# Kernel optimization log

Hardware: AMD Instinct MI355X
Metric: run time of the kernel (lower is better)

## Reference

```python
import jax, jax.numpy as jnp
import numpy as np

B, S, H = 2, 2048, 2048
NH, G = 16, 4
HD = H // NH  # 128


def setup_inputs() -> dict:
    key = jax.random.key(0)
    ks = jax.random.split(key, 9)
    sc = 0.02
    x = jax.random.normal(ks[0], (B, S, H), dtype=jnp.float32)
    # causal mask: 1.0 where j > i (masked), added as mask * -1e9 (matches torch code)
    causal_mask = jnp.triu(jnp.ones((S, S), dtype=jnp.float32), k=1)[None, None]
    Wq = jax.random.normal(ks[1], (H, H), dtype=jnp.float32) * sc
    bq = jnp.zeros((H,), dtype=jnp.float32)
    Wk = jax.random.normal(ks[2], (H, G * HD), dtype=jnp.float32) * sc
    bk = jnp.zeros((G * HD,), dtype=jnp.float32)
    Wv = jax.random.normal(ks[3], (H, G * HD), dtype=jnp.float32) * sc
    bv = jnp.zeros((G * HD,), dtype=jnp.float32)
    Wo = jax.random.normal(ks[4], (H, H), dtype=jnp.float32) * sc
    bo = jnp.zeros((H,), dtype=jnp.float32)
    return {"hidden_state": x, "causal_mask": causal_mask,
            "Wq": Wq, "bq": bq, "Wk": Wk, "bk": bk,
            "Wv": Wv, "bv": bv, "Wo": Wo, "bo": bo}


def reference(hidden_state, causal_mask, Wq, bq, Wk, bk, Wv, bv, Wo, bo):
    bsz, seq_len, _ = hidden_state.shape
    npg = NH // G  # query heads per KV group
    q = hidden_state @ Wq + bq                      # [B,S,H]
    k = hidden_state @ Wk + bk                      # [B,S,G*HD]
    v = hidden_state @ Wv + bv                      # [B,S,G*HD]
    # split heads; group query heads by KV group instead of repeating K/V
    q = q.reshape(bsz, seq_len, G, npg, HD).transpose(0, 2, 3, 1, 4)   # [B,G,npg,S,HD]
    k = k.reshape(bsz, seq_len, G, HD).transpose(0, 2, 1, 3)           # [B,G,S,HD]
    v = v.reshape(bsz, seq_len, G, HD).transpose(0, 2, 1, 3)           # [B,G,S,HD]
    scale = 1.0 / jnp.sqrt(jnp.float32(HD))
    scores = jnp.einsum('bgnsd,bgtd->bgnst', q, k) * scale             # [B,G,npg,S,S]
    scores = scores + causal_mask[:, :, None] * (-1e9)
    probs = jax.nn.softmax(scores, axis=-1)
    out = jnp.einsum('bgnst,bgtd->bgnsd', probs, v)                    # [B,G,npg,S,HD]
    out = out.transpose(0, 3, 1, 2, 4).reshape(bsz, seq_len, H)        # [B,S,H]
    return out @ Wo + bo
```

## Files before the change

kernel.cpp:

```cpp
#include <hip/hip_runtime.h>
#include <hip/hip_bf16.h>

#define B_   2
#define S_   2048
#define H_   2048
#define NH_  16
#define G_   4
#define HD_  128
#define NPG_ 4
#define MROWS_ (B_ * S_)
#define KVC_   (G_ * HD_)
#define NT_    (S_ / 64)
#define QSCALE_ 0.08838834764831845f

typedef __attribute__((ext_vector_type(8))) short bf16x8;
typedef __attribute__((ext_vector_type(4))) float f32x4;

__device__ __forceinline__ short f2bf_s(float f) {
    __hip_bfloat16 h = __float2bfloat16(f);
    short s; __builtin_memcpy(&s, &h, 2); return s;
}

__device__ __forceinline__ void gll16(const void* g, void* l) {
    __builtin_amdgcn_global_load_lds(
        (const __attribute__((address_space(1))) unsigned int*)g,
        (__attribute__((address_space(3))) unsigned int*)l, 16, 0, 0);
}

struct alignas(16) bf8pack { short s[8]; };
struct alignas(8)  s4pack  { short s[4]; };

__device__ __forceinline__ bf16x8 ld2x64(const short* p) {
    s4pack lo = *(const s4pack*)p;
    s4pack hi = *(const s4pack*)(p + 4);
    bf16x8 v;
    __builtin_memcpy(&v, &lo, 8);
    __builtin_memcpy((char*)&v + 8, &hi, 8);
    return v;
}

__device__ __forceinline__ void tile_transpose(
    const float* __restrict__ in, __hip_bfloat16* __restrict__ out,
    int R, int C, int bx, int by, int tid) {
    __shared__ short tile[32][33];
    int tx = tid & 31, ty0 = tid >> 5;
    #pragma unroll
    for (int i = 0; i < 32; i += 8)
        tile[ty0 + i][tx] = f2bf_s(in[(size_t)(by * 32 + ty0 + i) * C + bx * 32 + tx]);
    __syncthreads();
    #pragma unroll
    for (int i = 0; i < 32; i += 8) {
        short s = tile[tx][ty0 + i];
        __hip_bfloat16 h; __builtin_memcpy(&h, &s, 2);
        out[(size_t)(bx * 32 + ty0 + i) * R + by * 32 + tx] = h;
    }
}

__global__ __launch_bounds__(256) void prep(
    const float* __restrict__ x,  bf8pack* __restrict__ xb,
    const float* __restrict__ Wq, __hip_bfloat16* __restrict__ WqT,
    const float* __restrict__ Wk, __hip_bfloat16* __restrict__ WkT,
    const float* __restrict__ Wv, __hip_bfloat16* __restrict__ WvT,
    const float* __restrict__ Wo, __hip_bfloat16* __restrict__ WoT,
    const float* __restrict__ bq, const float* __restrict__ bk,
    const float* __restrict__ bv, float* __restrict__ bqkv) {
    const int bid = blockIdx.x, tid = threadIdx.x;
    if (bid < 4096) {
        int i = bid * 256 + tid;
        const float4* p = (const float4*)(x + (size_t)i * 8);
        float4 a = p[0], c = p[1];
        bf8pack o;
        o.s[0] = f2bf_s(a.x); o.s[1] = f2bf_s(a.y);
        o.s[2] = f2bf_s(a.z); o.s[3] = f2bf_s(a.w);
        o.s[4] = f2bf_s(c.x); o.s[5] = f2bf_s(c.y);
        o.s[6] = f2bf_s(c.z); o.s[7] = f2bf_s(c.w);
        xb[i] = o;
    } else if (bid < 8192) {
        int t = bid - 4096;
        tile_transpose(Wq, WqT, H_, H_, t & 63, t >> 6, tid);
    } else if (bid < 9216) {
        int t = bid - 8192;
        tile_transpose(Wk, WkT, H_, KVC_, t & 15, t >> 4, tid);
    } else if (bid < 10240) {
        int t = bid - 9216;
        tile_transpose(Wv, WvT, H_, KVC_, t & 15, t >> 4, tid);
    } else if (bid < 14336) {
        int t = bid - 10240;
        tile_transpose(Wo, WoT, H_, H_, t & 63, t >> 6, tid);
    } else {
        int i = (bid - 14336) * 256 + tid;
        if (i < 3072)
            bqkv[i] = (i < 2048) ? bq[i] : (i < 2560) ? bk[i - 2048] : bv[i - 2560];
    }
}

template <int BM>
__device__ __forceinline__ void gemm_core(
    const __hip_bfloat16* __restrict__ A,
    const __hip_bfloat16* __restrict__ Bt,
    const int K, const int bm, const int bn,
    short* __restrict__ As, short* __restrict__ Bs,
    f32x4 (* __restrict__ acc)[4])
{
    constexpr int MF  = BM / 32;
    constexpr int MH  = MF / 2;
    constexpr int AI  = BM / 64;
    constexpr int ASZ = BM * 64;
    constexpr int BSZ = 256 * 64;
    const int t0 = threadIdx.x;
    const int lane = t0 & 63, wave = t0 >> 6;
    const int l15 = lane & 15, quad = lane >> 4;
    const int lrow = lane >> 3, lcg = lane & 7;
    const int wm = (wave >> 2) * (BM / 2);
    const int wn = (wave & 3) * 64;
    const int nt = K >> 6;

    auto stage = [&](int ti) {
        const int kt = ti << 6;
        short* Ad = As + (ti & 1) * ASZ;
        short* Bd = Bs + (ti & 1) * BSZ;
        #pragma unroll
        for (int p = 0; p < AI; ++p) {
            const int r0 = wave * (AI * 8) + p * 8;
            const int row = r0 + lrow;
            gll16(A + (size_t)(bm + row) * K + kt + ((lcg ^ (row & 7)) << 3),
                  Ad + r0 * 64);
        }
        #pragma unroll
        for (int p = 0; p < 4; ++p) {
            const int r0 = wave * 32 + p * 8;
            const int row = r0 + lrow;
            gll16(Bt + (size_t)(bn + row) * K + kt + ((lcg ^ (row & 7)) << 3),
                  Bd + r0 * 64);
        }
    };

    stage(0);
    asm volatile("s_waitcnt vmcnt(0)" ::: "memory");
    asm volatile("s_barrier" ::: "memory");

    for (int t = 0; t < nt; ++t) {
        const short* Ab = As + (t & 1) * ASZ;
        const short* Bb = Bs + (t & 1) * BSZ;
        bf16x8 b01[2][2], b23[2][2], ah[MH][2];

        #pragma unroll
        for (int n = 0; n < 2; ++n) {
            const int rb = wn + n * 16 + l15;
            #pragma unroll
            for (int ks = 0; ks < 2; ++ks)
                b01[n][ks] = *(const bf16x8*)(Bb + rb * 64 +
                    (((ks * 4 + quad) ^ (rb & 7)) << 3));
        }
        #pragma unroll
        for (int i = 0; i < MH; ++i) {
            const int ra = wm + i * 16 + l15;
            #pragma unroll
            for (int ks = 0; ks < 2; ++ks)
                ah[i][ks] = *(const bf16x8*)(Ab + ra * 64 +
                    (((ks * 4 + quad) ^ (ra & 7)) << 3));
        }
        if (t + 1 < nt) stage(t + 1);
        asm volatile("s_barrier" ::: "memory");
        asm volatile("s_waitcnt lgkmcnt(0)" ::: "memory");
        __builtin_amdgcn_s_setprio(1);
        #pragma unroll
        for (int ks = 0; ks < 2; ++ks)
            #pragma unroll
            for (int i = 0; i < MH; ++i)
                #pragma unroll
                for (int n = 0; n < 2; ++n)
                    acc[i][n] = __builtin_amdgcn_mfma_f32_16x16x32_bf16(
                        ah[i][ks], b01[n][ks], acc[i][n], 0, 0, 0);
        __builtin_amdgcn_s_setprio(0);
        asm volatile("s_barrier" ::: "memory");

        #pragma unroll
        for (int n = 0; n < 2; ++n) {
            const int rb = wn + (2 + n) * 16 + l15;
            #pragma unroll
            for (int ks = 0; ks < 2; ++ks)
                b23[n][ks] = *(const bf16x8*)(Bb + rb * 64 +
                    (((ks * 4 + quad) ^ (rb & 7)) << 3));
        }
        asm volatile("s_barrier" ::: "memory");
        asm volatile("s_waitcnt lgkmcnt(0)" ::: "memory");
        __builtin_amdgcn_s_setprio(1);
        #pragma unroll
        for (int ks = 0; ks < 2; ++ks)
            #pragma unroll
            for (int i = 0; i < MH; ++i)
                #pragma unroll
                for (int n = 0; n < 2; ++n)
                    acc[i][2 + n] = __builtin_amdgcn_mfma_f32_16x16x32_bf16(
                        ah[i][ks], b23[n][ks], acc[i][2 + n], 0, 0, 0);
        __builtin_amdgcn_s_setprio(0);
        asm volatile("s_barrier" ::: "memory");

        #pragma unroll
        for (int i = 0; i < MH; ++i) {
            const int ra = wm + (MH + i) * 16 + l15;
            #pragma unroll
            for (int ks = 0; ks < 2; ++ks)
                ah[i][ks] = *(const bf16x8*)(Ab + ra * 64 +
                    (((ks * 4 + quad) ^ (ra & 7)) << 3));
        }
        asm volatile("s_barrier" ::: "memory");
        asm volatile("s_waitcnt lgkmcnt(0)" ::: "memory");
        __builtin_amdgcn_s_setprio(1);
        #pragma unroll
        for (int ks = 0; ks < 2; ++ks)
            #pragma unroll
            for (int i = 0; i < MH; ++i)
                #pragma unroll
                for (int n = 0; n < 2; ++n)
                    acc[MH + i][2 + n] = __builtin_amdgcn_mfma_f32_16x16x32_bf16(
                        ah[i][ks], b23[n][ks], acc[MH + i][2 + n], 0, 0, 0);
        __builtin_amdgcn_s_setprio(0);
        asm volatile("s_barrier" ::: "memory");

        __builtin_amdgcn_s_setprio(1);
        #pragma unroll
        for (int ks = 0; ks < 2; ++ks)
            #pragma unroll
            for (int i = 0; i < MH; ++i)
                #pragma unroll
                for (int n = 0; n < 2; ++n)
                    acc[MH + i][n] = __builtin_amdgcn_mfma_f32_16x16x32_bf16(
                        ah[i][ks], b01[n][ks], acc[MH + i][n], 0, 0, 0);
        __builtin_amdgcn_s_setprio(0);
        asm volatile("s_waitcnt vmcnt(0)" ::: "memory");
        asm volatile("s_barrier" ::: "memory");
    }
}

__global__ __launch_bounds__(512, 2) void gemm_qkv8(
    const __hip_bfloat16* __restrict__ A,
    const __hip_bfloat16* __restrict__ Bt,
    const float* __restrict__ bias,
    __hip_bfloat16* __restrict__ Qo,
    __hip_bfloat16* __restrict__ Ko,
    __hip_bfloat16* __restrict__ VtG) {
    __shared__ __align__(16) short As[2 * 256 * 64];
    __shared__ __align__(16) short Bs[2 * 256 * 64];
    const int bid = blockIdx.x;
    const int s = (bid & 7) * 24 + (bid >> 3);
    const int bm = (s & 15) * 256, bn = (s >> 4) * 256;

    f32x4 acc[8][4] = {};
    gemm_core<256>(A, Bt, H_, bm, bn, As, Bs, acc);

    const int t = threadIdx.x;
    const int lane = t & 63, wave = t >> 6;
    const int l15 = lane & 15, quad = lane >> 4;
    const int wm = (wave >> 2) * 128, wn = (wave & 3) * 64;

    #pragma unroll
    for (int i = 0; i < 8; ++i) {
        int row0 = bm + wm + i * 16 + quad * 4;
        #pragma unroll
        for (int j = 0; j < 4; ++j) {
            int c0 = bn + wn + j * 16;
            int colg = c0 + l15;
            float bv = bias[colg];
            if (c0 < 2048) {
                #pragma unroll
                for (int r = 0; r < 4; ++r)
                    Qo[(size_t)(row0 + r) * H_ + colg] =
                        __float2bfloat16((acc[i][j][r] + bv) * QSCALE_);
            } else if (c0 < 2560) {
                #pragma unroll
                for (int r = 0; r < 4; ++r)
                    Ko[(size_t)(row0 + r) * KVC_ + (colg - 2048)] =
                        __float2bfloat16(acc[i][j][r] + bv);
            } else {
                int coll = colg - 2560;
                short s4v[4];
                #pragma unroll
                for (int r = 0; r < 4; ++r) s4v[r] = f2bf_s(acc[i][j][r] + bv);
                *(uint2*)(&VtG[(size_t)coll * MROWS_ + row0]) = *(uint2*)s4v;
            }
        }
    }
}

__global__ __launch_bounds__(512, 2) void gemm_out8(
    const __hip_bfloat16* __restrict__ A,
    const __hip_bfloat16* __restrict__ Bt,
    const float* __restrict__ bias,
    float* __restrict__ C) {
    __shared__ __align__(16) short As[2 * 128 * 64];
    __shared__ __align__(16) short Bs[2 * 256 * 64];
    const int bid = blockIdx.x;
    const int s = (bid & 7) * 32 + (bid >> 3);
    const int bm = (s & 31) * 128, bn = (s >> 5) * 256;

    f32x4 acc[4][4] = {};
    gemm_core<128>(A, Bt, H_, bm, bn, As, Bs, acc);

    const int t = threadIdx.x;
    const int lane = t & 63, wave = t >> 6;
    const int l15 = lane & 15, quad = lane >> 4;
    const int wm = (wave >> 2) * 64, wn = (wave & 3) * 64;

    #pragma unroll
    for (int i = 0; i < 4; ++i) {
        int row0 = bm + wm + i * 16 + quad * 4;
        #pragma unroll
        for (int j = 0; j < 4; ++j) {
            int col = bn + wn + j * 16 + l15;
            float bv = bias[col];
            #pragma unroll
            for (int r = 0; r < 4; ++r)
                C[(size_t)(row0 + r) * H_ + col] = acc[i][j][r] + bv;
        }
    }
}

__global__ __launch_bounds__(256, 2) void attn_causal_gqa(
    const __hip_bfloat16* __restrict__ Q,
    const __hip_bfloat16* __restrict__ K,
    const __hip_bfloat16* __restrict__ VtG,
    __hip_bfloat16* __restrict__ O) {
    __shared__ short KsL[2][64 * 128];
    __shared__ short VtL[128 * 64];
    __shared__ short Ps[4][2][16 * 76];

    const int h  = blockIdx.x;
    const int b  = h >> 4;
    const int hh = h & 15;
    const int g  = hh >> 2;
    const int qb1 = blockIdx.y;
    const int qb2 = NT_ - 1 - qb1;

    const int t = threadIdx.x;
    const int lane = t & 63, wave = t >> 6;
    const int l15 = lane & 15, quad = lane >> 4;
    const int swz = l15 & 7;

    const __hip_bfloat16* Qb = Q + (size_t)b * S_ * H_ + hh * HD_;
    const __hip_bfloat16* Kb = K + (size_t)b * S_ * KVC_ + g * HD_;
    const __hip_bfloat16* Vg = VtG + (size_t)g * HD_ * MROWS_ + b * S_;

    auto stageK = [&](int tile) {
        short* kd = &KsL[tile & 1][0];
        #pragma unroll
        for (int p = 0; p < 4; ++p) {
            int R0 = wave * 16 + p * 4;
            int row = R0 + (lane >> 4);
            int cg = ((lane & 15) ^ (row & 7)) * 8;
            gll16(Kb + (size_t)(tile * 64 + row) * KVC_ + cg, &kd[R0 * 128]);
        }
    };
    auto stageV = [&](int tile) {
        #pragma unroll
        for (int p = 0; p < 4; ++p) {
            int R0 = wave * 32 + p * 8;
            int row = R0 + (lane >> 3);
            int cg = ((lane & 7) ^ (row & 7)) * 8;
            gll16(Vg + (size_t)row * MROWS_ + tile * 64 + cg, &VtL[R0 * 64]);
        }
    };

    bf16x8 aq1[4], aq2[4];
    {
        const int qr1 = qb1 * 64 + wave * 16 + l15;
        const int qr2 = qb2 * 64 + wave * 16 + l15;
        #pragma unroll
        for (int kk = 0; kk < 4; ++kk) {
            aq1[kk] = *(const bf16x8*)(Qb + (size_t)qr1 * H_ + kk * 32 + quad * 8);
            aq2[kk] = *(const bf16x8*)(Qb + (size_t)qr2 * H_ + kk * 32 + quad * 8);
        }
    }

    f32x4 o1[8] = {}, o2[8] = {};
    float lp1 = 0.f, lp2 = 0.f;
    const int qrow_loc = wave * 16 + l15;

    stageK(0);

    for (int tile = 0; tile <= qb2; ++tile) {
        const bool do1 = (tile <= qb1);
        const bool last = (tile == qb2);

        stageV(tile);
        if (!last) stageK(tile + 1);

        if (!last) asm volatile("s_waitcnt vmcnt(8)" ::: "memory");
        else       asm volatile("s_waitcnt vmcnt(4)" ::: "memory");
        asm volatile("s_barrier" ::: "memory");

        const short* kb = &KsL[tile & 1][0];

        f32x4 s2[4] = {}, s1[4] = {};
        #pragma unroll
        for (int kk = 0; kk < 4; ++kk) {
            bf16x8 bk[4];
            #pragma unroll
            for (int nt = 0; nt < 4; ++nt)
                bk[nt] = *(const bf16x8*)(
                    &kb[(nt * 16 + l15) * 128 + (((kk * 4 + quad) ^ swz) * 8)]);
            #pragma unroll
            for (int nt = 0; nt < 4; ++nt)
                s2[nt] = __builtin_amdgcn_mfma_f32_16x16x32_bf16(
                    bk[nt], aq2[kk], s2[nt], 0, 0, 0);
            if (do1) {
                #pragma unroll
                for (int nt = 0; nt < 4; ++nt)
                    s1[nt] = __builtin_amdgcn_mfma_f32_16x16x32_bf16(
                        bk[nt], aq1[kk], s1[nt], 0, 0, 0);
            }
        }

        __asm__ volatile("" ::: "memory");
        short* P2 = &Ps[wave][1][0];
        {
            const bool m2 = (tile == qb2);
            #pragma unroll
            for (int nt = 0; nt < 4; ++nt) {
                s4pack pk;
                #pragma unroll
                for (int r = 0; r < 4; ++r) {
                    float p = __expf(s2[nt][r]);
                    if (m2 && (nt * 16 + quad * 4 + r > qrow_loc)) p = 0.f;
                    lp2 += p;
                    pk.s[r] = f2bf_s(p);
                }
                *(s4pack*)&P2[l15 * 76 + nt * 16 + quad * 4] = pk;
            }
        }
        short* P1 = &Ps[wave][0][0];
        if (do1) {
            const bool m1 = (tile == qb1);
            #pragma unroll
            for (int nt = 0; nt < 4; ++nt) {
                s4pack pk;
                #pragma unroll
                for (int r = 0; r < 4; ++r) {
                    float p = __expf(s1[nt][r]);
                    if (m1 && (nt * 16 + quad * 4 + r > qrow_loc)) p = 0.f;
                    lp1 += p;
                    pk.s[r] = f2bf_s(p);
                }
                *(s4pack*)&P1[l15 * 76 + nt * 16 + quad * 4] = pk;
            }
        }
        __asm__ volatile("" ::: "memory");

        if (!last) asm volatile("s_waitcnt vmcnt(4)" ::: "memory");
        else       asm volatile("s_waitcnt vmcnt(0)" ::: "memory");
        asm volatile("s_barrier" ::: "memory");

        #pragma unroll
        for (int ks = 0; ks < 2; ++ks) {
            bf16x8 ap2 = ld2x64(&P2[l15 * 76 + ks * 32 + quad * 8]);
            bf16x8 ap1;
            if (do1) ap1 = ld2x64(&P1[l15 * 76 + ks * 32 + quad * 8]);
            #pragma unroll
            for (int n2 = 0; n2 < 8; ++n2) {
                bf16x8 bv = *(const bf16x8*)(
                    &VtL[(n2 * 16 + l15) * 64 + (((ks * 4 + quad) ^ swz) * 8)]);
                o2[n2] = __builtin_amdgcn_mfma_f32_16x16x32_bf16(
                    ap2, bv, o2[n2], 0, 0, 0);
                if (do1)
                    o1[n2] = __builtin_amdgcn_mfma_f32_16x16x32_bf16(
                        ap1, bv, o1[n2], 0, 0, 0);
            }
        }
        asm volatile("s_barrier" ::: "memory");
    }

    float L1 = lp1, L2 = lp2;
    L1 += __shfl_xor(L1, 16); L2 += __shfl_xor(L2, 16);
    L1 += __shfl_xor(L1, 32); L2 += __shfl_xor(L2, 32);
    #pragma unroll
    for (int r = 0; r < 4; ++r) {
        float i1 = 1.f / __shfl(L1, quad * 4 + r);
        float i2 = 1.f / __shfl(L2, quad * 4 + r);
        int s1r = qb1 * 64 + wave * 16 + quad * 4 + r;
        int s2r = qb2 * 64 + wave * 16 + quad * 4 + r;
        #pragma unroll
        for (int n2 = 0; n2 < 8; ++n2) {
            int d = n2 * 16 + l15;
            O[((size_t)b * S_ + s1r) * H_ + hh * HD_ + d] = __float2bfloat16(o1[n2][r] * i1);
            O[((size_t)b * S_ + s2r) * H_ + hh * HD_ + d] = __float2bfloat16(o2[n2][r] * i2);
        }
    }
}

extern "C" void kernel_launch(void* const* d_in, const int* in_sizes, int n_in,
                              void* d_out, int out_size, void* d_ws, size_t ws_size,
                              hipStream_t stream) {
    const float* x  = (const float*)d_in[0];
    const float* Wq = (const float*)d_in[2];
    const float* bq = (const float*)d_in[3];
    const float* Wk = (const float*)d_in[4];
    const float* bk = (const float*)d_in[5];
    const float* Wv = (const float*)d_in[6];
    const float* bv = (const float*)d_in[7];
    const float* Wo = (const float*)d_in[8];
    const float* bo = (const float*)d_in[9];
    float* out = (float*)d_out;

    char* ws = (char*)d_ws;
    const size_t MB = 1024 * 1024;
    __hip_bfloat16* xb   = (__hip_bfloat16*)(ws);
    __hip_bfloat16* WT   = (__hip_bfloat16*)(ws + 16 * MB);
    __hip_bfloat16* Kws  = (__hip_bfloat16*)(ws + 28 * MB);
    __hip_bfloat16* VtG  = (__hip_bfloat16*)(ws + 32 * MB);
    __hip_bfloat16* WoT  = (__hip_bfloat16*)(ws + 36 * MB);
    float*          bqkv = (float*)         (ws + 44 * MB);
    __hip_bfloat16* Aws  = (__hip_bfloat16*)(ws);
    __hip_bfloat16* Qbuf = (__hip_bfloat16*)d_out;

    prep<<<14348, 256, 0, stream>>>(
        x, (bf8pack*)xb,
        Wq, WT,
        Wk, WT + (size_t)2048 * H_,
        Wv, WT + (size_t)2560 * H_,
        Wo, WoT,
        bq, bk, bv, bqkv);

    gemm_qkv8<<<192, 512, 0, stream>>>(xb, WT, bqkv, Qbuf, Kws, VtG);

    attn_causal_gqa<<<dim3(B_ * NH_, NT_ / 2), 256, 0, stream>>>(Qbuf, Kws, VtG, Aws);

    gemm_out8<<<256, 512, 0, stream>>>(Aws, WoT, bo, out);
}
```

Before: 311.7 us.

## Prefetch two K-tiles ahead, retile QKV GEMM to 256x192, vectorize weight transpose

```diff
diff --git a/kernel.cpp b/kernel.cpp
--- a/kernel.cpp
+++ b/kernel.cpp
@@ -39,21 +39,30 @@
     return v;
 }
 
-__device__ __forceinline__ void tile_transpose(
+__device__ __forceinline__ void tile_transpose64(
     const float* __restrict__ in, __hip_bfloat16* __restrict__ out,
     int R, int C, int bx, int by, int tid) {
-    __shared__ short tile[32][33];
-    int tx = tid & 31, ty0 = tid >> 5;
+    __shared__ short tile[64][66];
+    const int r = tid >> 2, c0 = (tid & 3) * 16;
+    const float4* src = (const float4*)(in + (size_t)(by * 64 + r) * C + bx * 64 + c0);
+    float4 f0 = src[0], f1 = src[1], f2 = src[2], f3 = src[3];
+    short* tp = &tile[r][c0];
+    tp[0]  = f2bf_s(f0.x); tp[1]  = f2bf_s(f0.y);
+    tp[2]  = f2bf_s(f0.z); tp[3]  = f2bf_s(f0.w);
+    tp[4]  = f2bf_s(f1.x); tp[5]  = f2bf_s(f1.y);
+    tp[6]  = f2bf_s(f1.z); tp[7]  = f2bf_s(f1.w);
+    tp[8]  = f2bf_s(f2.x); tp[9]  = f2bf_s(f2.y);
+    tp[10] = f2bf_s(f2.z); tp[11] = f2bf_s(f2.w);
+    tp[12] = f2bf_s(f3.x); tp[13] = f2bf_s(f3.y);
+    tp[14] = f2bf_s(f3.z); tp[15] = f2bf_s(f3.w);
+    __syncthreads();
+    const int j = tid >> 2, i0 = (tid & 3) * 16;
+    short pk[16];
     #pragma unroll
-    for (int i = 0; i < 32; i += 8)
-        tile[ty0 + i][tx] = f2bf_s(in[(size_t)(by * 32 + ty0 + i) * C + bx * 32 + tx]);
-    __syncthreads();
-    #pragma unroll
-    for (int i = 0; i < 32; i += 8) {
-        short s = tile[tx][ty0 + i];
-        __hip_bfloat16 h; __builtin_memcpy(&h, &s, 2);
-        out[(size_t)(bx * 32 + ty0 + i) * R + by * 32 + tx] = h;
-    }
+    for (int i = 0; i < 16; ++i) pk[i] = tile[i0 + i][j];
+    __hip_bfloat16* dst = out + (size_t)(bx * 64 + j) * R + by * 64 + i0;
+    *(uint4*)(dst)     = *(uint4*)(pk);
+    *(uint4*)(dst + 8) = *(uint4*)(pk + 8);
 }
 
 __global__ __launch_bounds__(256) void prep(
@@ -75,44 +84,45 @@
         o.s[4] = f2bf_s(c.x); o.s[5] = f2bf_s(c.y);
         o.s[6] = f2bf_s(c.z); o.s[7] = f2bf_s(c.w);
         xb[i] = o;
-    } else if (bid < 8192) {
+    } else if (bid < 5120) {
         int t = bid - 4096;
-        tile_transpose(Wq, WqT, H_, H_, t & 63, t >> 6, tid);
-    } else if (bid < 9216) {
-        int t = bid - 8192;
-        tile_transpose(Wk, WkT, H_, KVC_, t & 15, t >> 4, tid);
-    } else if (bid < 10240) {
-        int t = bid - 9216;
-        tile_transpose(Wv, WvT, H_, KVC_, t & 15, t >> 4, tid);
-    } else if (bid < 14336) {
-        int t = bid - 10240;
-        tile_transpose(Wo, WoT, H_, H_, t & 63, t >> 6, tid);
+        tile_transpose64(Wq, WqT, H_, H_, t & 31, t >> 5, tid);
+    } else if (bid < 5376) {
+        int t = bid - 5120;
+        tile_transpose64(Wk, WkT, H_, KVC_, t & 7, t >> 3, tid);
+    } else if (bid < 5632) {
+        int t = bid - 5376;
+        tile_transpose64(Wv, WvT, H_, KVC_, t & 7, t >> 3, tid);
+    } else if (bid < 6656) {
+        int t = bid - 5632;
+        tile_transpose64(Wo, WoT, H_, H_, t & 31, t >> 5, tid);
     } else {
-        int i = (bid - 14336) * 256 + tid;
+        int i = (bid - 6656) * 256 + tid;
         if (i < 3072)
             bqkv[i] = (i < 2048) ? bq[i] : (i < 2560) ? bk[i - 2048] : bv[i - 2560];
     }
 }
 
-template <int BM>
+template <int BM, int NF>
 __device__ __forceinline__ void gemm_core(
     const __hip_bfloat16* __restrict__ A,
     const __hip_bfloat16* __restrict__ Bt,
     const int K, const int bm, const int bn,
     short* __restrict__ As, short* __restrict__ Bs,
-    f32x4 (* __restrict__ acc)[4])
+    f32x4 (* __restrict__ acc)[NF])
 {
-    constexpr int MF  = BM / 32;
-    constexpr int MH  = MF / 2;
+    constexpr int MH  = BM / 64;
     constexpr int AI  = BM / 64;
+    constexpr int NB2 = NF - 2;
+    constexpr int STG = AI + NF;
     constexpr int ASZ = BM * 64;
-    constexpr int BSZ = 256 * 64;
+    constexpr int BSZ = 64 * NF * 64;
     const int t0 = threadIdx.x;
     const int lane = t0 & 63, wave = t0 >> 6;
     const int l15 = lane & 15, quad = lane >> 4;
     const int lrow = lane >> 3, lcg = lane & 7;
     const int wm = (wave >> 2) * (BM / 2);
-    const int wn = (wave & 3) * 64;
+    const int wn = (wave & 3) * (16 * NF);
     const int nt = K >> 6;
 
     auto stage = [&](int ti) {
@@ -127,29 +137,36 @@
                   Ad + r0 * 64);
         }
         #pragma unroll
-        for (int p = 0; p < 4; ++p) {
-            const int r0 = wave * 32 + p * 8;
+        for (int p = 0; p < NF; ++p) {
+            const int r0 = wave * (NF * 8) + p * 8;
             const int row = r0 + lrow;
             gll16(Bt + (size_t)(bn + row) * K + kt + ((lcg ^ (row & 7)) << 3),
                   Bd + r0 * 64);
         }
     };
 
-    stage(0);
-    asm volatile("s_waitcnt vmcnt(0)" ::: "memory");
+    auto waitcnt_stg = [&]() {
+        if constexpr (STG == 7)      asm volatile("s_waitcnt vmcnt(7)" ::: "memory");
+        else if constexpr (STG == 6) asm volatile("s_waitcnt vmcnt(6)" ::: "memory");
+        else if constexpr (STG == 8) asm volatile("s_waitcnt vmcnt(8)" ::: "memory");
+        else                         asm volatile("s_waitcnt vmcnt(0)" ::: "memory");
+    };
+
+    stage(0); stage(1);
+    waitcnt_stg();
     asm volatile("s_barrier" ::: "memory");
 
     for (int t = 0; t < nt; ++t) {
         const short* Ab = As + (t & 1) * ASZ;
         const short* Bb = Bs + (t & 1) * BSZ;
-        bf16x8 b01[2][2], b23[2][2], ah[MH][2];
+        bf16x8 bg1[2][2], bg2[NB2][2], ah[MH][2];
 
         #pragma unroll
         for (int n = 0; n < 2; ++n) {
             const int rb = wn + n * 16 + l15;
             #pragma unroll
             for (int ks = 0; ks < 2; ++ks)
-                b01[n][ks] = *(const bf16x8*)(Bb + rb * 64 +
+                bg1[n][ks] = *(const bf16x8*)(Bb + rb * 64 +
                     (((ks * 4 + quad) ^ (rb & 7)) << 3));
         }
         #pragma unroll
@@ -160,7 +177,6 @@
                 ah[i][ks] = *(const bf16x8*)(Ab + ra * 64 +
                     (((ks * 4 + quad) ^ (ra & 7)) << 3));
         }
-        if (t + 1 < nt) stage(t + 1);
         asm volatile("s_barrier" ::: "memory");
         asm volatile("s_waitcnt lgkmcnt(0)" ::: "memory");
         __builtin_amdgcn_s_setprio(1);
@@ -171,16 +187,16 @@
                 #pragma unroll
                 for (int n = 0; n < 2; ++n)
                     acc[i][n] = __builtin_amdgcn_mfma_f32_16x16x32_bf16(
-                        ah[i][ks], b01[n][ks], acc[i][n], 0, 0, 0);
+                        ah[i][ks], bg1[n][ks], acc[i][n], 0, 0, 0);
         __builtin_amdgcn_s_setprio(0);
         asm volatile("s_barrier" ::: "memory");
 
         #pragma unroll
-        for (int n = 0; n < 2; ++n) {
+        for (int n = 0; n < NB2; ++n) {
             const int rb = wn + (2 + n) * 16 + l15;
             #pragma unroll
             for (int ks = 0; ks < 2; ++ks)
-                b23[n][ks] = *(const bf16x8*)(Bb + rb * 64 +
+                bg2[n][ks] = *(const bf16x8*)(Bb + rb * 64 +
                     (((ks * 4 + quad) ^ (rb & 7)) << 3));
         }
         asm volatile("s_barrier" ::: "memory");
@@ -191,9 +207,9 @@
             #pragma unroll
             for (int i = 0; i < MH; ++i)
                 #pragma unroll
-                for (int n = 0; n < 2; ++n)
+                for (int n = 0; n < NB2; ++n)
                     acc[i][2 + n] = __builtin_amdgcn_mfma_f32_16x16x32_bf16(
-                        ah[i][ks], b23[n][ks], acc[i][2 + n], 0, 0, 0);
+                        ah[i][ks], bg2[n][ks], acc[i][2 + n], 0, 0, 0);
         __builtin_amdgcn_s_setprio(0);
         asm volatile("s_barrier" ::: "memory");
 
@@ -213,12 +229,13 @@
             #pragma unroll
             for (int i = 0; i < MH; ++i)
                 #pragma unroll
-                for (int n = 0; n < 2; ++n)
+                for (int n = 0; n < NB2; ++n)
                     acc[MH + i][2 + n] = __builtin_amdgcn_mfma_f32_16x16x32_bf16(
-                        ah[i][ks], b23[n][ks], acc[MH + i][2 + n], 0, 0, 0);
+                        ah[i][ks], bg2[n][ks], acc[MH + i][2 + n], 0, 0, 0);
         __builtin_amdgcn_s_setprio(0);
         asm volatile("s_barrier" ::: "memory");
 
+        if (t + 2 < nt) stage(t + 2);
         __builtin_amdgcn_s_setprio(1);
         #pragma unroll
         for (int ks = 0; ks < 2; ++ks)
@@ -227,10 +244,16 @@
                 #pragma unroll
                 for (int n = 0; n < 2; ++n)
                     acc[MH + i][n] = __builtin_amdgcn_mfma_f32_16x16x32_bf16(
-                        ah[i][ks], b01[n][ks], acc[MH + i][n], 0, 0, 0);
+                        ah[i][ks], bg1[n][ks], acc[MH + i][n], 0, 0, 0);
         __builtin_amdgcn_s_setprio(0);
-        asm volatile("s_waitcnt vmcnt(0)" ::: "memory");
-        asm volatile("s_barrier" ::: "memory");
+
+        if (t + 2 < nt) {
+            waitcnt_stg();
+            asm volatile("s_barrier" ::: "memory");
+        } else if (t + 1 < nt) {
+            asm volatile("s_waitcnt vmcnt(0)" ::: "memory");
+            asm volatile("s_barrier" ::: "memory");
+        }
     }
 }
 
@@ -242,24 +265,24 @@
     __hip_bfloat16* __restrict__ Ko,
     __hip_bfloat16* __restrict__ VtG) {
     __shared__ __align__(16) short As[2 * 256 * 64];
-    __shared__ __align__(16) short Bs[2 * 256 * 64];
+    __shared__ __align__(16) short Bs[2 * 192 * 64];
     const int bid = blockIdx.x;
-    const int s = (bid & 7) * 24 + (bid >> 3);
-    const int bm = (s & 15) * 256, bn = (s >> 4) * 256;
-
-    f32x4 acc[8][4] = {};
-    gemm_core<256>(A, Bt, H_, bm, bn, As, Bs, acc);
+    const int s = (bid & 7) * 32 + (bid >> 3);
+    const int bm = (s & 15) * 256, bn = (s >> 4) * 192;
+
+    f32x4 acc[8][3] = {};
+    gemm_core<256, 3>(A, Bt, H_, bm, bn, As, Bs, acc);
 
     const int t = threadIdx.x;
     const int lane = t & 63, wave = t >> 6;
     const int l15 = lane & 15, quad = lane >> 4;
-    const int wm = (wave >> 2) * 128, wn = (wave & 3) * 64;
+    const int wm = (wave >> 2) * 128, wn = (wave & 3) * 48;
 
     #pragma unroll
     for (int i = 0; i < 8; ++i) {
         int row0 = bm + wm + i * 16 + quad * 4;
         #pragma unroll
-        for (int j = 0; j < 4; ++j) {
+        for (int j = 0; j < 3; ++j) {
             int c0 = bn + wn + j * 16;
             int colg = c0 + l15;
             float bv = bias[colg];
@@ -296,7 +319,7 @@
     const int bm = (s & 31) * 128, bn = (s >> 5) * 256;
 
     f32x4 acc[4][4] = {};
-    gemm_core<128>(A, Bt, H_, bm, bn, As, Bs, acc);
+    gemm_core<128, 4>(A, Bt, H_, bm, bn, As, Bs, acc);
 
     const int t = threadIdx.x;
     const int lane = t & 63, wave = t >> 6;
@@ -513,7 +536,7 @@
     __hip_bfloat16* Aws  = (__hip_bfloat16*)(ws);
     __hip_bfloat16* Qbuf = (__hip_bfloat16*)d_out;
 
-    prep<<<14348, 256, 0, stream>>>(
+    prep<<<6669, 256, 0, stream>>>(
         x, (bf8pack*)xb,
         Wq, WT,
         Wk, WT + (size_t)2048 * H_,
@@ -521,7 +544,7 @@
         Wo, WoT,
         bq, bk, bv, bqkv);
 
-    gemm_qkv8<<<192, 512, 0, stream>>>(xb, WT, bqkv, Qbuf, Kws, VtG);
+    gemm_qkv8<<<256, 512, 0, stream>>>(xb, WT, bqkv, Qbuf, Kws, VtG);
 
     attn_causal_gqa<<<dim3(B_ * NH_, NT_ / 2), 256, 0, stream>>>(Qbuf, Kws, VtG, Aws);
 
```

New measurement: 303.8 us. -2.5%, faster.
